# Performance work log

Hardware: AMD Instinct MI355X
Metric: run time of the kernel (lower is better)

Reference implementation:

```python
import jax, jax.numpy as jnp
import numpy as np

# Static problem dims (match LSS defaults: camC=64, downsample=8, 224x480 imgs, nuScenes grid)
B, N, D, FH, FW, C = 2, 6, 60, 28, 60, 64
NX, NY, NZ = 200, 200, 1
NUM_SEG = NX * NY * NZ * B
IMG_H, IMG_W = 224, 480
EPS = 1e-5


def setup_inputs() -> dict:
    key = jax.random.key(0)
    k1, k2 = jax.random.split(key)
    feats = jax.random.normal(k1, (B * N, C, FH, FW), jnp.float32)
    depth = jax.random.normal(k2, (B * N, D, FH, FW), jnp.float32)

    # frustum exactly as LSS.create_frustum: (D, fH, fW, 3) with (u, v, d)
    ds = np.arange(1.0, 61.0, 1.0, dtype=np.float32).reshape(-1, 1, 1) * np.ones((1, FH, FW), np.float32)
    xs = np.linspace(0.0, IMG_W - 1, FW, dtype=np.float32).reshape(1, 1, FW) * np.ones((D, FH, 1), np.float32)
    ys = np.linspace(0.0, IMG_H - 1, FH, dtype=np.float32).reshape(1, FH, 1) * np.ones((D, 1, FW), np.float32)
    frustum = jnp.asarray(np.stack([xs, ys, ds], -1))

    # realistic lidar2img = K @ E per camera (invertible, points land in the 100m grid)
    fx = fy = 250.0; cx = 240.0; cy = 112.0
    K = np.array([[fx, 0, cx, 0], [0, fy, cy, 0], [0, 0, 1, 0], [0, 0, 0, 1]], np.float32)
    mats = []
    for b in range(B):
        row = []
        for cam in range(N):
            th = 2.0 * np.pi * cam / N
            right = np.array([-np.sin(th), np.cos(th), 0.0])
            down = np.array([0.0, 0.0, -1.0])
            fwd = np.array([np.cos(th), np.sin(th), 0.0])
            Rm = np.stack([right, down, fwd], 0)
            t = np.array([0.0, 0.0, 1.5])
            E = np.eye(4, dtype=np.float32)
            E[:3, :3] = Rm
            E[:3, 3] = -Rm @ t
            row.append(K @ E)
        mats.append(row)
    lidar2img = jnp.asarray(np.array(mats, np.float32))

    # gen_dx_bx for xbound/ybound [-50,50,0.5], zbound [-10,10,20]
    dx = jnp.array([0.5, 0.5, 20.0], jnp.float32)
    bx = jnp.array([-50.0 + 0.25, -50.0 + 0.25, -10.0 + 10.0], jnp.float32)
    return {"feats": feats, "depth": depth, "lidar2img": lidar2img,
            "frustum": frustum, "dx": dx, "bx": bx}


def reference(feats, depth, lidar2img, frustum, dx, bx):
    # depth-weighted outer product: (BN,C,D,h,w)
    x = jax.nn.softmax(depth, axis=1)[:, None] * feats[:, :, None]
    # -> (B, N, D, h, w, C)
    x = x.reshape(B, N, C, D, FH, FW).transpose(0, 1, 3, 4, 5, 2)

    # get_geometry: lift frustum pixels to lidar frame
    p = jnp.concatenate([
        frustum[..., :2] * jnp.maximum(frustum[..., 2:3], EPS),
        frustum[..., 2:3],
        jnp.ones_like(frustum[..., :1]),
    ], -1)  # (D,h,w,4)
    img2lidar = jnp.linalg.inv(lidar2img)  # (B,N,4,4)
    geom = jnp.einsum('bnij,dhwj->bndhwi', img2lidar, p)[..., :3]  # (B,N,D,h,w,3)

    # voxel_pooling: quantize (torch .long() truncates toward zero, as does astype)
    g = ((geom - (bx - dx / 2.0)) / dx).astype(jnp.int32).reshape(-1, 3)  # (Nprime,3)
    xf = x.reshape(-1, C)  # (Nprime, C)
    batch_ix = jnp.repeat(jnp.arange(B, dtype=jnp.int32), xf.shape[0] // B)

    kept = ((g[:, 0] >= 0) & (g[:, 0] < NX) &
            (g[:, 1] >= 0) & (g[:, 1] < NY) &
            (g[:, 2] >= 0) & (g[:, 2] < NZ))
    ranks = g[:, 0] * (NY * NZ * B) + g[:, 1] * (NZ * B) + g[:, 2] * B + batch_ix
    seg = jnp.where(kept, ranks, NUM_SEG)  # dump bucket for out-of-range points

    # sort + QuickCumsum segmented reduction == per-voxel segment sum
    sums = jax.ops.segment_sum(xf * kept[:, None].astype(xf.dtype), seg,
                               num_segments=NUM_SEG + 1)[:-1]  # (NX*NY*NZ*B, C)

    # scatter into (B, C, NZ, NX, NY) then cat-unbind over z -> (B, NZ*C, NX, NY)
    final = sums.reshape(NX, NY, NZ, B, C).transpose(3, 2, 4, 0, 1)  # (B,NZ,C,NX,NY)
    return final.reshape(B, NZ * C, NX, NY)
```

## Files before the change

### kernel.cpp

```cpp
#include <hip/hip_runtime.h>
#include <math.h>

#define B_   2
#define N_   6
#define D_   60
#define FH_  28
#define FW_  60
#define C_   64
#define NX_  200
#define NY_  200
#define HW_  (FH_*FW_)
#define NPIX_ (B_*N_*HW_)
#define DSPLIT 15
#define DCHUNK (D_/DSPLIT)
#define ACC_N4 ((B_*NX_*NY_*C_)/4)
#define NFILLB 1024
#define NSMBLK ((NPIX_+255)/256)
#define NTTILE ((HW_+63)/64)

__global__ void k_pre(const float* __restrict__ l2i, float* __restrict__ minv_out,
                      float4* __restrict__ acc4,
                      const float* __restrict__ depth, float* __restrict__ wt,
                      const float* __restrict__ feats, float* __restrict__ ft) {
#pragma clang fp contract(off)
    __shared__ float tile[64][65];
    if (blockIdx.x < NFILLB) {
        if (blockIdx.x == 0 && threadIdx.x < B_ * N_) {
            int m = threadIdx.x;
            float a[4][4];
            for (int r = 0; r < 4; r++)
                for (int c = 0; c < 4; c++)
                    a[r][c] = l2i[m * 16 + r * 4 + c];
            int ipiv[4];
            for (int j = 0; j < 4; j++) {
                int jp = j; float amax = fabsf(a[j][j]);
                for (int i = j + 1; i < 4; i++) {
                    float v = fabsf(a[i][j]);
                    if (v > amax) { amax = v; jp = i; }
                }
                ipiv[j] = jp;
                if (jp != j)
                    for (int c = 0; c < 4; c++) { float t = a[j][c]; a[j][c] = a[jp][c]; a[jp][c] = t; }
                if (a[j][j] != 0.0f) {
                    float rcp = 1.0f / a[j][j];
                    for (int i = j + 1; i < 4; i++) a[i][j] = a[i][j] * rcp;
                }
                for (int k = j + 1; k < 4; k++) {
                    float temp = -a[j][k];
                    if (temp != 0.0f)
                        for (int i = j + 1; i < 4; i++)
                            a[i][k] = fmaf(a[i][j], temp, a[i][k]);
                }
            }
            float bmat[4][4];
            for (int r = 0; r < 4; r++)
                for (int c = 0; c < 4; c++) bmat[r][c] = (r == c) ? 1.0f : 0.0f;
            for (int j = 0; j < 4; j++) {
                int jp = ipiv[j];
                if (jp != j)
                    for (int c = 0; c < 4; c++) { float t = bmat[j][c]; bmat[j][c] = bmat[jp][c]; bmat[jp][c] = t; }
            }
            for (int c = 0; c < 4; c++)
                for (int k = 0; k < 4; k++) {
                    float bk = bmat[k][c];
                    if (bk != 0.0f)
                        for (int i = k + 1; i < 4; i++)
                            bmat[i][c] = fmaf(-bk, a[i][k], bmat[i][c]);
                }
            float dinv[4];
            for (int k = 0; k < 4; k++) dinv[k] = 1.0f / a[k][k];
            for (int c = 0; c < 4; c++)
                for (int k = 3; k >= 0; k--) {
                    float bk = bmat[k][c];
                    if (bk != 0.0f) {
                        bk = bk * dinv[k];
                        bmat[k][c] = bk;
                        for (int i = 0; i < k; i++)
                            bmat[i][c] = fmaf(-bk, a[i][k], bmat[i][c]);
                    }
                }
            for (int r = 0; r < 4; r++)
                for (int c = 0; c < 4; c++)
                    minv_out[m * 16 + r * 4 + c] = bmat[r][c];
        }
        float4 z = make_float4(0.f, 0.f, 0.f, 0.f);
        int stride = NFILLB * blockDim.x;
        for (int i = blockIdx.x * blockDim.x + threadIdx.x; i < ACC_N4; i += stride)
            acc4[i] = z;
    } else if (blockIdx.x < NFILLB + NSMBLK) {
        int p = (blockIdx.x - NFILLB) * blockDim.x + threadIdx.x;
        if (p >= NPIX_) return;
        int bn = p / HW_;
        int hw = p - bn * HW_;
        const float* dptr = depth + (size_t)bn * D_ * HW_ + hw;
        float v[D_];
        float mx = -1e30f;
        #pragma unroll
        for (int d = 0; d < D_; d++) { v[d] = dptr[(size_t)d * HW_]; mx = fmaxf(mx, v[d]); }
        float s = 0.f;
        #pragma unroll
        for (int d = 0; d < D_; d++) { v[d] = expf(v[d] - mx); s += v[d]; }
        float is = 1.f / s;
        float* o = wt + (size_t)p * D_;
        #pragma unroll
        for (int d = 0; d < D_; d++) o[d] = v[d] * is;
    } else {
        int bid = blockIdx.x - NFILLB - NSMBLK;
        int bn = bid / NTTILE;
        int p0 = (bid % NTTILE) * 64;
        int tx = threadIdx.x & 63;
        int ty = threadIdx.x >> 6;
        const float* src = feats + (size_t)bn * C_ * HW_;
        #pragma unroll
        for (int k = 0; k < 16; k++) {
            int c = ty * 16 + k;
            int p = p0 + tx;
            if (p < HW_) tile[c][tx] = src[(size_t)c * HW_ + p];
        }
        __syncthreads();
        float* dst = ft + (size_t)bn * HW_ * C_;
        #pragma unroll
        for (int k = 0; k < 16; k++) {
            int pl = ty * 16 + k;
            int p = p0 + pl;
            if (p < HW_) dst[(size_t)p * C_ + tx] = tile[tx][pl];
        }
    }
}

__global__ void k_scatter4(const float* __restrict__ frustum,
                           const float* __restrict__ minv,
                           const float* __restrict__ wt,
                           const float* __restrict__ ft,
                           const float* __restrict__ dxp,
                           const float* __restrict__ bxp,
                           float* __restrict__ acc) {
#pragma clang fp contract(off)
    int gtid = blockIdx.x * blockDim.x + threadIdx.x;
    int wvid = gtid >> 6;
    int lane = threadIdx.x & 63;
    if (wvid >= B_ * N_ * FW_ * DSPLIT) return;
    int dq = wvid % DSPLIT;
    int w  = (wvid / DSPLIT) % FW_;
    int bn = wvid / (DSPLIT * FW_);
    int b  = bn / N_;
    int bnbase = bn * HW_;
    int d0 = dq * DCHUNK;

    float ftreg[FH_];
    #pragma unroll
    for (int h = 0; h < FH_; h++)
        ftreg[h] = ft[(size_t)(bnbase + h * FW_ + w) * C_ + lane];

    float u = frustum[w * 3 + 0];
    float v = 0.f;
    float4 w4 = make_float4(0.f, 0.f, 0.f, 0.f);
    if (lane < FH_) {
        v = frustum[((size_t)lane * FW_ + w) * 3 + 1];
        int pix = bnbase + lane * FW_ + w;
        w4 = *reinterpret_cast<const float4*>(&wt[(size_t)pix * D_ + d0]);
    }
    const float* M = minv + (size_t)bn * 16;
    float M0 = M[0], M1 = M[1], M2 = M[2],  M3 = M[3];
    float M4 = M[4], M5 = M[5], M6 = M[6],  M7 = M[7];
    float M8 = M[8], M9 = M[9], M10 = M[10], M11 = M[11];
    float dx0 = dxp[0], dx1 = dxp[1], dx2 = dxp[2];
    float lb0 = bxp[0] - dx0 * 0.5f;
    float lb1 = bxp[1] - dx1 * 0.5f;
    float lb2 = bxp[2] - dx2 * 0.5f;

    #pragma unroll
    for (int k = 0; k < DCHUNK; k++) {
        int d = d0 + k;
        float mywt = (k == 0) ? w4.x : (k == 1) ? w4.y : (k == 2) ? w4.z : w4.w;
        int myenc = -1;
        if (lane < FH_) {
            float dd = (float)(d + 1);
            float dm = fmaxf(dd, 1e-5f);
            float p0 = u * dm;
            float p1 = v * dm;
            float p2 = dd;
            float x0 = M0 * p0, x1 = M1 * p1, x2 = M2 * p2, x3 = M3 * 1.0f;
            float gx = (x0 + x1) + (x2 + x3);
            float y0 = M4 * p0, y1 = M5 * p1, y2 = M6 * p2, y3 = M7 * 1.0f;
            float gy = (y0 + y1) + (y2 + y3);
            float z0 = M8 * p0, z1 = M9 * p1, z2 = M10 * p2, z3 = M11 * 1.0f;
            float gz = (z0 + z1) + (z2 + z3);
            float qx = (gx - lb0) / dx0;
            float qy = (gy - lb1) / dx1;
            float qz = (gz - lb2) / dx2;
            int ix = (int)qx;
            int iy = (int)qy;
            int iz = (int)qz;
            if (ix >= 0 && ix < NX_ && iy >= 0 && iy < NY_ && iz == 0)
                myenc = (((b * NX_) + ix) * NY_ + iy) * C_;
        }

        unsigned long long processed = 0;
        for (int j = 0; j < FH_; ++j) {
            if (processed & (1ull << j)) continue;
            int e = __shfl(myenc, j, 64);
            unsigned long long mm = __ballot(lane < FH_ && myenc == e);
            processed |= mm;
            if (e < 0) continue;
            float s = 0.f;
            #pragma unroll
            for (int h = 0; h < FH_; h++) {
                float wh = __shfl(mywt, h, 64);
                s = fmaf(((mm >> h) & 1ull) ? wh : 0.0f, ftreg[h], s);
            }
            atomicAdd(&acc[(size_t)e + lane], s);
        }
    }
}

__global__ void k_out(const float* __restrict__ acc, float* __restrict__ out) {
    __shared__ float tile[64][65];
    int b = blockIdx.y;
    int p0 = blockIdx.x * 64;
    int tx = threadIdx.x & 63;
    int ty = threadIdx.x >> 6;
    const float* src = acc + (size_t)b * (NX_ * NY_) * C_;
    #pragma unroll
    for (int k = 0; k < 16; k++) {
        int pl = ty * 16 + k;
        tile[pl][tx] = src[(size_t)(p0 + pl) * C_ + tx];
    }
    __syncthreads();
    float* dst = out + (size_t)b * C_ * (NX_ * NY_);
    #pragma unroll
    for (int k = 0; k < 16; k++) {
        int c = ty * 16 + k;
        dst[(size_t)c * (NX_ * NY_) + p0 + tx] = tile[tx][c];
    }
}

extern "C" void kernel_launch(void* const* d_in, const int* in_sizes, int n_in,
                              void* d_out, int out_size, void* d_ws, size_t ws_size,
                              hipStream_t stream) {
    const float* feats = (const float*)d_in[0];
    const float* depth = (const float*)d_in[1];
    const float* l2i   = (const float*)d_in[2];
    const float* frust = (const float*)d_in[3];
    const float* dx    = (const float*)d_in[4];
    const float* bx    = (const float*)d_in[5];
    float* out = (float*)d_out;

    char* ws = (char*)d_ws;
    float* minv = (float*)ws;
    float* wt  = (float*)(ws + 2048);
    float* ft  = (float*)(ws + 2048 + 4838400);
    float* acc = (float*)(ws + 2048 + 4838400 + 5160960);

    k_pre<<<NFILLB + NSMBLK + B_ * N_ * NTTILE, 256, 0, stream>>>(
        l2i, minv, (float4*)acc, depth, wt, feats, ft);
    int nwaves = B_ * N_ * FW_ * DSPLIT;
    k_scatter4<<<(nwaves * 64 + 255) / 256, 256, 0, stream>>>(frust, minv, wt, ft, dx, bx, acc);
    k_out<<<dim3((NX_ * NY_) / 64, B_), 256, 0, stream>>>(acc, out);
}
```

Before: 56.29 us.

## Fuse pre, scatter and output stages into one cooperative persistent kernel

Merges the three launches (softmax/transpose/zero-fill, atomic scatter, output transpose) into a single cooperative kernel that uses grid-wide syncs between phases and grid-stride loops sized to occupancy. The aim is to remove the gaps between kernel launches and the launch overhead. In exchange it adds grid.sync costs, caps the grid at 1024 persistent blocks, and adds host-side attribute and occupancy queries on every call. The old three-kernel path is kept as a fallback when cooperative launch is unavailable.

New measurement: 209.8 us. +272.8%, slower.

```diff
diff --git a/kernel.cpp b/kernel.cpp
--- a/kernel.cpp
+++ b/kernel.cpp
@@ -1,5 +1,8 @@
 #include <hip/hip_runtime.h>
+#include <hip/hip_cooperative_groups.h>
 #include <math.h>
+
+namespace cg = cooperative_groups;
 
 #define B_   2
 #define N_   6
@@ -14,132 +17,123 @@
 #define DSPLIT 15
 #define DCHUNK (D_/DSPLIT)
 #define ACC_N4 ((B_*NX_*NY_*C_)/4)
-#define NFILLB 1024
 #define NSMBLK ((NPIX_+255)/256)
 #define NTTILE ((HW_+63)/64)
-
-__global__ void k_pre(const float* __restrict__ l2i, float* __restrict__ minv_out,
-                      float4* __restrict__ acc4,
-                      const float* __restrict__ depth, float* __restrict__ wt,
-                      const float* __restrict__ feats, float* __restrict__ ft) {
+#define NTRB   (B_*N_*NTTILE)
+#define NROLE  (NSMBLK+NTRB)
+#define NWAVES (B_*N_*FW_*DSPLIT)
+#define NOUTT  (B_*(NX_*NY_/64))
+
+__device__ void inv12(const float* __restrict__ l2i, float* __restrict__ minv, int m) {
 #pragma clang fp contract(off)
-    __shared__ float tile[64][65];
-    if (blockIdx.x < NFILLB) {
-        if (blockIdx.x == 0 && threadIdx.x < B_ * N_) {
-            int m = threadIdx.x;
-            float a[4][4];
-            for (int r = 0; r < 4; r++)
-                for (int c = 0; c < 4; c++)
-                    a[r][c] = l2i[m * 16 + r * 4 + c];
-            int ipiv[4];
-            for (int j = 0; j < 4; j++) {
-                int jp = j; float amax = fabsf(a[j][j]);
-                for (int i = j + 1; i < 4; i++) {
-                    float v = fabsf(a[i][j]);
-                    if (v > amax) { amax = v; jp = i; }
-                }
-                ipiv[j] = jp;
-                if (jp != j)
-                    for (int c = 0; c < 4; c++) { float t = a[j][c]; a[j][c] = a[jp][c]; a[jp][c] = t; }
-                if (a[j][j] != 0.0f) {
-                    float rcp = 1.0f / a[j][j];
-                    for (int i = j + 1; i < 4; i++) a[i][j] = a[i][j] * rcp;
-                }
-                for (int k = j + 1; k < 4; k++) {
-                    float temp = -a[j][k];
-                    if (temp != 0.0f)
-                        for (int i = j + 1; i < 4; i++)
-                            a[i][k] = fmaf(a[i][j], temp, a[i][k]);
-                }
+    float a[4][4];
+    for (int r = 0; r < 4; r++)
+        for (int c = 0; c < 4; c++)
+            a[r][c] = l2i[m * 16 + r * 4 + c];
+    int ipiv[4];
+    for (int j = 0; j < 4; j++) {
+        int jp = j; float amax = fabsf(a[j][j]);
+        for (int i = j + 1; i < 4; i++) {
+            float v = fabsf(a[i][j]);
+            if (v > amax) { amax = v; jp = i; }
+        }
+        ipiv[j] = jp;
+        if (jp != j)
+            for (int c = 0; c < 4; c++) { float t = a[j][c]; a[j][c] = a[jp][c]; a[jp][c] = t; }
+        if (a[j][j] != 0.0f) {
+            float rcp = 1.0f / a[j][j];
+            for (int i = j + 1; i < 4; i++) a[i][j] = a[i][j] * rcp;
+        }
+        for (int k = j + 1; k < 4; k++) {
+            float temp = -a[j][k];
+            if (temp != 0.0f)
+                for (int i = j + 1; i < 4; i++)
+                    a[i][k] = fmaf(a[i][j], temp, a[i][k]);
+        }
+    }
+    float bmat[4][4];
+    for (int r = 0; r < 4; r++)
+        for (int c = 0; c < 4; c++) bmat[r][c] = (r == c) ? 1.0f : 0.0f;
+    for (int j = 0; j < 4; j++) {
+        int jp = ipiv[j];
+        if (jp != j)
+            for (int c = 0; c < 4; c++) { float t = bmat[j][c]; bmat[j][c] = bmat[jp][c]; bmat[jp][c] = t; }
+    }
+    for (int c = 0; c < 4; c++)
+        for (int k = 0; k < 4; k++) {
+            float bk = bmat[k][c];
+            if (bk != 0.0f)
+                for (int i = k + 1; i < 4; i++)
+                    bmat[i][c] = fmaf(-bk, a[i][k], bmat[i][c]);
+        }
+    float dinv[4];
+    for (int k = 0; k < 4; k++) dinv[k] = 1.0f / a[k][k];
+    for (int c = 0; c < 4; c++)
+        for (int k = 3; k >= 0; k--) {
+            float bk = bmat[k][c];
+            if (bk != 0.0f) {
+                bk = bk * dinv[k];
+                bmat[k][c] = bk;
+                for (int i = 0; i < k; i++)
+                    bmat[i][c] = fmaf(-bk, a[i][k], bmat[i][c]);
             }
-            float bmat[4][4];
-            for (int r = 0; r < 4; r++)
-                for (int c = 0; c < 4; c++) bmat[r][c] = (r == c) ? 1.0f : 0.0f;
-            for (int j = 0; j < 4; j++) {
-                int jp = ipiv[j];
-                if (jp != j)
-                    for (int c = 0; c < 4; c++) { float t = bmat[j][c]; bmat[j][c] = bmat[jp][c]; bmat[jp][c] = t; }
-            }
-            for (int c = 0; c < 4; c++)
-                for (int k = 0; k < 4; k++) {
-                    float bk = bmat[k][c];
-                    if (bk != 0.0f)
-                        for (int i = k + 1; i < 4; i++)
-                            bmat[i][c] = fmaf(-bk, a[i][k], bmat[i][c]);
-                }
-            float dinv[4];
-            for (int k = 0; k < 4; k++) dinv[k] = 1.0f / a[k][k];
-            for (int c = 0; c < 4; c++)
-                for (int k = 3; k >= 0; k--) {
-                    float bk = bmat[k][c];
-                    if (bk != 0.0f) {
-                        bk = bk * dinv[k];
-                        bmat[k][c] = bk;
-                        for (int i = 0; i < k; i++)
-                            bmat[i][c] = fmaf(-bk, a[i][k], bmat[i][c]);
-                    }
-                }
-            for (int r = 0; r < 4; r++)
-                for (int c = 0; c < 4; c++)
-                    minv_out[m * 16 + r * 4 + c] = bmat[r][c];
-        }
-        float4 z = make_float4(0.f, 0.f, 0.f, 0.f);
-        int stride = NFILLB * blockDim.x;
-        for (int i = blockIdx.x * blockDim.x + threadIdx.x; i < ACC_N4; i += stride)
-            acc4[i] = z;
-    } else if (blockIdx.x < NFILLB + NSMBLK) {
-        int p = (blockIdx.x - NFILLB) * blockDim.x + threadIdx.x;
-        if (p >= NPIX_) return;
-        int bn = p / HW_;
-        int hw = p - bn * HW_;
-        const float* dptr = depth + (size_t)bn * D_ * HW_ + hw;
-        float v[D_];
-        float mx = -1e30f;
-        #pragma unroll
-        for (int d = 0; d < D_; d++) { v[d] = dptr[(size_t)d * HW_]; mx = fmaxf(mx, v[d]); }
-        float s = 0.f;
-        #pragma unroll
-        for (int d = 0; d < D_; d++) { v[d] = expf(v[d] - mx); s += v[d]; }
-        float is = 1.f / s;
-        float* o = wt + (size_t)p * D_;
-        #pragma unroll
-        for (int d = 0; d < D_; d++) o[d] = v[d] * is;
-    } else {
-        int bid = blockIdx.x - NFILLB - NSMBLK;
-        int bn = bid / NTTILE;
-        int p0 = (bid % NTTILE) * 64;
-        int tx = threadIdx.x & 63;
-        int ty = threadIdx.x >> 6;
-        const float* src = feats + (size_t)bn * C_ * HW_;
-        #pragma unroll
-        for (int k = 0; k < 16; k++) {
-            int c = ty * 16 + k;
-            int p = p0 + tx;
-            if (p < HW_) tile[c][tx] = src[(size_t)c * HW_ + p];
-        }
-        __syncthreads();
-        float* dst = ft + (size_t)bn * HW_ * C_;
-        #pragma unroll
-        for (int k = 0; k < 16; k++) {
-            int pl = ty * 16 + k;
-            int p = p0 + pl;
-            if (p < HW_) dst[(size_t)p * C_ + tx] = tile[tx][pl];
-        }
-    }
-}
-
-__global__ void k_scatter4(const float* __restrict__ frustum,
-                           const float* __restrict__ minv,
-                           const float* __restrict__ wt,
-                           const float* __restrict__ ft,
-                           const float* __restrict__ dxp,
-                           const float* __restrict__ bxp,
-                           float* __restrict__ acc) {
+        }
+    for (int r = 0; r < 4; r++)
+        for (int c = 0; c < 4; c++)
+            minv[m * 16 + r * 4 + c] = bmat[r][c];
+}
+
+__device__ void softmax_block(const float* __restrict__ depth, float* __restrict__ wt,
+                              int smblk, int tid) {
+    int p = smblk * 256 + tid;
+    if (p >= NPIX_) return;
+    int bn = p / HW_;
+    int hw = p - bn * HW_;
+    const float* dptr = depth + (size_t)bn * D_ * HW_ + hw;
+    float v[D_];
+    float mx = -1e30f;
+    #pragma unroll
+    for (int d = 0; d < D_; d++) { v[d] = dptr[(size_t)d * HW_]; mx = fmaxf(mx, v[d]); }
+    float s = 0.f;
+    #pragma unroll
+    for (int d = 0; d < D_; d++) { v[d] = expf(v[d] - mx); s += v[d]; }
+    float is = 1.f / s;
+    float* o = wt + (size_t)p * D_;
+    #pragma unroll
+    for (int d = 0; d < D_; d++) o[d] = v[d] * is;
+}
+
+__device__ void tfeat_block(const float* __restrict__ feats, float* __restrict__ ft,
+                            float (*tile)[65], int bid, int tid) {
+    int bn = bid / NTTILE;
+    int p0 = (bid % NTTILE) * 64;
+    int tx = tid & 63;
+    int ty = tid >> 6;
+    const float* src = feats + (size_t)bn * C_ * HW_;
+    #pragma unroll
+    for (int k = 0; k < 16; k++) {
+        int c = ty * 16 + k;
+        int p = p0 + tx;
+        if (p < HW_) tile[c][tx] = src[(size_t)c * HW_ + p];
+    }
+    __syncthreads();
+    float* dst = ft + (size_t)bn * HW_ * C_;
+    #pragma unroll
+    for (int k = 0; k < 16; k++) {
+        int pl = ty * 16 + k;
+        int p = p0 + pl;
+        if (p < HW_) dst[(size_t)p * C_ + tx] = tile[tx][pl];
+    }
+}
+
+__device__ void scatter_wave(const float* __restrict__ frustum,
+                             const float* __restrict__ minv,
+                             const float* __restrict__ wt,
+                             const float* __restrict__ ft,
+                             const float* __restrict__ dxp,
+                             const float* __restrict__ bxp,
+                             float* __restrict__ acc, int wvid, int lane) {
 #pragma clang fp contract(off)
-    int gtid = blockIdx.x * blockDim.x + threadIdx.x;
-    int wvid = gtid >> 6;
-    int lane = threadIdx.x & 63;
-    if (wvid >= B_ * N_ * FW_ * DSPLIT) return;
     int dq = wvid % DSPLIT;
     int w  = (wvid / DSPLIT) % FW_;
     int bn = wvid / (DSPLIT * FW_);
@@ -195,7 +189,6 @@
             if (ix >= 0 && ix < NX_ && iy >= 0 && iy < NY_ && iz == 0)
                 myenc = (((b * NX_) + ix) * NY_ + iy) * C_;
         }
-
         unsigned long long processed = 0;
         for (int j = 0; j < FH_; ++j) {
             if (processed & (1ull << j)) continue;
@@ -214,12 +207,12 @@
     }
 }
 
-__global__ void k_out(const float* __restrict__ acc, float* __restrict__ out) {
-    __shared__ float tile[64][65];
-    int b = blockIdx.y;
-    int p0 = blockIdx.x * 64;
-    int tx = threadIdx.x & 63;
-    int ty = threadIdx.x >> 6;
+__device__ void out_tile(const float* __restrict__ acc, float* __restrict__ out,
+                         float (*tile)[65], int vt, int tid) {
+    int tx = tid & 63;
+    int ty = tid >> 6;
+    int b = vt / (NX_ * NY_ / 64);
+    int p0 = (vt % (NX_ * NY_ / 64)) * 64;
     const float* src = acc + (size_t)b * (NX_ * NY_) * C_;
     #pragma unroll
     for (int k = 0; k < 16; k++) {
@@ -233,6 +226,86 @@
         int c = ty * 16 + k;
         dst[(size_t)c * (NX_ * NY_) + p0 + tx] = tile[tx][c];
     }
+}
+
+__global__ void __launch_bounds__(256, 4)
+k_fused(const float* __restrict__ l2i, float* __restrict__ minv,
+        float4* __restrict__ acc4,
+        const float* __restrict__ depth, float* __restrict__ wt,
+        const float* __restrict__ feats, float* __restrict__ ft,
+        const float* __restrict__ frustum,
+        const float* __restrict__ dxp, const float* __restrict__ bxp,
+        float* __restrict__ acc, float* __restrict__ out) {
+    cg::grid_group grid = cg::this_grid();
+    __shared__ float tile[64][65];
+    int tid = threadIdx.x;
+    int nb = gridDim.x;
+
+    if (blockIdx.x < NSMBLK) {
+        softmax_block(depth, wt, blockIdx.x, tid);
+    } else if (blockIdx.x < NROLE) {
+        tfeat_block(feats, ft, tile, blockIdx.x - NSMBLK, tid);
+    } else {
+        if (blockIdx.x == NROLE && tid < B_ * N_) inv12(l2i, minv, tid);
+        float4 z = make_float4(0.f, 0.f, 0.f, 0.f);
+        int base = (blockIdx.x - NROLE) * 256 + tid;
+        int stride = (nb - NROLE) * 256;
+        for (int i = base; i < ACC_N4; i += stride) acc4[i] = z;
+    }
+
+    grid.sync();
+
+    {
+        int lane = tid & 63;
+        int gw = blockIdx.x * 4 + (tid >> 6);
+        for (int wvid = gw; wvid < NWAVES; wvid += nb * 4)
+            scatter_wave(frustum, minv, wt, ft, dxp, bxp, acc, wvid, lane);
+    }
+
+    grid.sync();
+
+    for (int vt = blockIdx.x; vt < NOUTT; vt += nb) {
+        __syncthreads();
+        out_tile(acc, out, tile, vt, tid);
+    }
+}
+
+__global__ void k_pre(const float* __restrict__ l2i, float* __restrict__ minv_out,
+                      float4* __restrict__ acc4,
+                      const float* __restrict__ depth, float* __restrict__ wt,
+                      const float* __restrict__ feats, float* __restrict__ ft) {
+    __shared__ float tile[64][65];
+    if (blockIdx.x < 1024) {
+        if (blockIdx.x == 0 && threadIdx.x < B_ * N_) inv12(l2i, minv_out, threadIdx.x);
+        float4 z = make_float4(0.f, 0.f, 0.f, 0.f);
+        int stride = 1024 * 256;
+        for (int i = blockIdx.x * 256 + threadIdx.x; i < ACC_N4; i += stride)
+            acc4[i] = z;
+    } else if (blockIdx.x < 1024 + NSMBLK) {
+        softmax_block(depth, wt, blockIdx.x - 1024, threadIdx.x);
+    } else {
+        tfeat_block(feats, ft, tile, blockIdx.x - 1024 - NSMBLK, threadIdx.x);
+    }
+}
+
+__global__ void k_scatter4(const float* __restrict__ frustum,
+                           const float* __restrict__ minv,
+                           const float* __restrict__ wt,
+                           const float* __restrict__ ft,
+                           const float* __restrict__ dxp,
+                           const float* __restrict__ bxp,
+                           float* __restrict__ acc) {
+    int gtid = blockIdx.x * blockDim.x + threadIdx.x;
+    int wvid = gtid >> 6;
+    int lane = threadIdx.x & 63;
+    if (wvid >= NWAVES) return;
+    scatter_wave(frustum, minv, wt, ft, dxp, bxp, acc, wvid, lane);
+}
+
+__global__ void k_out(const float* __restrict__ acc, float* __restrict__ out) {
+    __shared__ float tile[64][65];
+    int vt = blockIdx.y * (NX_ * NY_ / 64) + blockIdx.x;
+    out_tile(acc, out, tile, vt, threadIdx.x);
 }
 
 extern "C" void kernel_launch(void* const* d_in, const int* in_sizes, int n_in,
@@ -251,10 +324,30 @@
     float* wt  = (float*)(ws + 2048);
     float* ft  = (float*)(ws + 2048 + 4838400);
     float* acc = (float*)(ws + 2048 + 4838400 + 5160960);
-
-    k_pre<<<NFILLB + NSMBLK + B_ * N_ * NTTILE, 256, 0, stream>>>(
-        l2i, minv, (float4*)acc, depth, wt, feats, ft);
-    int nwaves = B_ * N_ * FW_ * DSPLIT;
-    k_scatter4<<<(nwaves * 64 + 255) / 256, 256, 0, stream>>>(frust, minv, wt, ft, dx, bx, acc);
-    k_out<<<dim3((NX_ * NY_) / 64, B_), 256, 0, stream>>>(acc, out);
-}
+    float4* acc4 = (float4*)acc;
+
+    int dev = 0;
+    hipGetDevice(&dev);
+    int coop = 0;
+    hipDeviceGetAttribute(&coop, hipDeviceAttributeCooperativeLaunch, dev);
+    int perCU = 0;
+    hipOccupancyMaxActiveBlocksPerMultiprocessor(&perCU, k_fused, 256, 0);
+    int nCU = 0;
+    hipDeviceGetAttribute(&nCU, hipDeviceAttributeMultiprocessorCount, dev);
+    long maxB = (long)perCU * (long)nCU;
+    int nb = (int)(maxB < 1024 ? maxB : 1024);
+
+    if (coop && nb >= NROLE + 64) {
+        void* args[] = { (void*)&l2i, (void*)&minv, (void*)&acc4,
+                         (void*)&depth, (void*)&wt,
+                         (void*)&feats, (void*)&ft,
+                         (void*)&frust, (void*)&dx, (void*)&bx,
+                         (void*)&acc, (void*)&out };
+        hipLaunchCooperativeKernel((const void*)k_fused, dim3(nb), dim3(256),
+                                   args, 0, stream);
+    } else {
+        k_pre<<<1024 + NSMBLK + NTRB, 256, 0, stream>>>(l2i, minv, acc4, depth, wt, feats, ft);
+        k_scatter4<<<(NWAVES * 64 + 255) / 256, 256, 0, stream>>>(frust, minv, wt, ft, dx, bx, acc);
+        k_out<<<dim3(NX_ * NY_ / 64, B_), 256, 0, stream>>>(acc, out);
+    }
+}
```
